# Performance work log

Measured on AMD Instinct MI355X. Metric: run time of the kernel, lower is better.

## Reference

```python
import jax, jax.numpy as jnp
import numpy as np

IN_F = 4096
OUT_F = 4096
GS = 128              # group_size
GC = IN_F // GS       # group_count = 32
PACK = 8              # int4 values per int32


def setup_inputs() -> dict:
    key = jax.random.key(0)
    k1, k2, k3, k4, k5 = jax.random.split(key, 5)
    x = jax.random.normal(k1, (4, 2048, IN_F), dtype=jnp.float32)
    # packed int4 weights: (out_features, in_features // 8), nibbles in low->high bits
    qweight = jax.random.randint(k2, (OUT_F, IN_F // PACK), -(2**31), 2**31 - 1, dtype=jnp.int32)
    scales = jax.random.uniform(k3, (GC, OUT_F), dtype=jnp.float32) * 0.01
    qzeros = jax.random.randint(k4, (GC, OUT_F), 0, 16, dtype=jnp.int32)
    bias = jax.random.normal(k5, (OUT_F,), dtype=jnp.float32) * 0.01
    return {"x": x, "qweight": qweight, "scales": scales, "qzeros": qzeros, "bias": bias}


def _dequantize(qweight, scales, qzeros):
    # unpack 8 nibbles per int32 along last dim (shifts 0,4,...,28), as in _unpack_int4_last_dim
    shifts = jnp.arange(0, 32, 4, dtype=jnp.int32)  # [8]
    w_int = ((qweight[:, :, None] >> shifts) & 15)  # (OUT, IN//8, 8)
    w_int = w_int.reshape(OUT_F, IN_F).astype(jnp.float32)  # (OUT, IN)
    gid = jnp.arange(IN_F) // GS  # (IN,) group id per input channel
    z = qzeros.astype(jnp.float32)[gid].T   # (OUT, IN)
    s = scales[gid].T                        # (OUT, IN)
    return (w_int - z) * s                   # (OUT, IN)


def reference(x, qweight, scales, qzeros, bias):
    W = _dequantize(qweight, scales, qzeros)          # (OUT, IN)
    # F.linear: y = x @ W^T + b
    return jnp.einsum('bsi,oi->bso', x, W) + bias
```

## Files before the change

### kernel.cpp

```cpp
#include <hip/hip_runtime.h>
#include <hip/hip_bf16.h>
#include <stdint.h>

#define IN_F 4096
#define OUT_F 4096
#define M_TOTAL 8192
#define NKT 64

typedef __hip_bfloat16 bf16;
typedef __attribute__((ext_vector_type(8))) short bf16x8;
typedef __attribute__((ext_vector_type(4))) float f32x4;

__global__ __launch_bounds__(256) void prep(const int* __restrict__ qweight,
                                            const float* __restrict__ scales,
                                            const int* __restrict__ qzeros,
                                            bf16* __restrict__ Wb,
                                            const float* __restrict__ x,
                                            bf16* __restrict__ Xb) {
    int b = blockIdx.x;
    if (b < 8192) {
        int idx = b * 256 + threadIdx.x;
        int o = idx >> 9;
        int j = idx & 511;
        int g = j >> 4;
        int qw = qweight[idx];
        float s = scales[g * OUT_F + o];
        float z = (float)qzeros[g * OUT_F + o];
        union { bf16 h[8]; uint4 q; } out;
#pragma unroll
        for (int k = 0; k < 8; ++k) {
            float w = (float)((qw >> (4 * k)) & 15);
            out.h[k] = __float2bfloat16((w - z) * s);
        }
        *reinterpret_cast<uint4*>(Wb + ((size_t)o * IN_F + j * 8)) = out.q;
    } else {
        int idx = (b - 8192) * 256 + threadIdx.x;
        const float4* p = reinterpret_cast<const float4*>(x) + (size_t)idx * 2;
        float4 a = p[0], c = p[1];
        union { bf16 h[8]; uint4 q; } o;
        o.h[0] = __float2bfloat16(a.x); o.h[1] = __float2bfloat16(a.y);
        o.h[2] = __float2bfloat16(a.z); o.h[3] = __float2bfloat16(a.w);
        o.h[4] = __float2bfloat16(c.x); o.h[5] = __float2bfloat16(c.y);
        o.h[6] = __float2bfloat16(c.z); o.h[7] = __float2bfloat16(c.w);
        reinterpret_cast<uint4*>(Xb)[idx] = o.q;
    }
}


__device__ __forceinline__ void gload16(const bf16* g, char* l) {
    __builtin_amdgcn_global_load_lds(
        (const __attribute__((address_space(1))) void*)g,
        (__attribute__((address_space(3))) void*)l, 16, 0, 0);
}

__device__ __forceinline__ void stage_half(const bf16* __restrict__ Gt,
                                           char* ldsb, int wave, int lane) {
    const int slog8 = ((lane & 7) ^ (lane >> 3)) * 8;
#pragma unroll
    for (int j = 0; j < 2; ++j) {
        int r = wave * 16 + j * 8 + (lane >> 3);
        gload16(Gt + (size_t)r * IN_F + slog8, ldsb + (wave * 2 + j) * 1024);
    }
}

#define BARRIER() do { asm volatile("" ::: "memory"); \
                       __builtin_amdgcn_s_barrier();  \
                       asm volatile("" ::: "memory"); } while (0)
#define LGKM0()   asm volatile("s_waitcnt lgkmcnt(0)" ::: "memory")
#define VMCNT6()  asm volatile("s_waitcnt vmcnt(6)" ::: "memory")
#define VMCNT0()  asm volatile("s_waitcnt vmcnt(0)" ::: "memory")

#define LDA_SET(DST, BUF, MH) do {                                              \
  _Pragma("unroll") for (int m4 = 0; m4 < 4; ++m4)                              \
  _Pragma("unroll") for (int kk = 0; kk < 2; ++kk)                              \
    DST[m4][kk] = *reinterpret_cast<const bf16x8*>(sm + (BUF) * 65536           \
        + (((MH) * 128 + wr * 64 + m4 * 16 + l15) << 7)                         \
        + ((((kk << 2) + lq) ^ l7) << 4));                                      \
} while (0)

#define LDB_SET(DST, BUF, NH) do {                                              \
  _Pragma("unroll") for (int n2 = 0; n2 < 2; ++n2)                              \
  _Pragma("unroll") for (int kk = 0; kk < 2; ++kk)                              \
    DST[n2][kk] = *reinterpret_cast<const bf16x8*>(sm + (BUF) * 65536 + 32768   \
        + (((NH) * 128 + wc * 32 + n2 * 16 + l15) << 7)                         \
        + ((((kk << 2) + lq) ^ l7) << 4));                                      \
} while (0)

#define MMA_Q(AF, BFR, MH, NH) do {                                             \
  __builtin_amdgcn_s_setprio(1);                                                \
  _Pragma("unroll") for (int m4 = 0; m4 < 4; ++m4)                              \
  _Pragma("unroll") for (int n2 = 0; n2 < 2; ++n2)                              \
  _Pragma("unroll") for (int kk = 0; kk < 2; ++kk)                              \
    acc[(MH) * 4 + m4][(NH) * 2 + n2] = __builtin_amdgcn_mfma_f32_16x16x32_bf16(\
        AF[m4][kk], BFR[n2][kk], acc[(MH) * 4 + m4][(NH) * 2 + n2], 0, 0, 0);   \
  __builtin_amdgcn_s_setprio(0);                                                \
} while (0)

__global__ __launch_bounds__(512, 2) void gemm256(const bf16* __restrict__ A,
                                                  const bf16* __restrict__ B,
                                                  const float* __restrict__ bias,
                                                  float* __restrict__ C) {
    extern __shared__ char sm[];
    const int tid  = threadIdx.x;
    const int wave = tid >> 6;
    const int lane = tid & 63;
    const int wr   = wave >> 2;
    const int wc   = wave & 3;
    const int l15  = lane & 15;
    const int lq   = lane >> 4;
    const int l7   = lane & 7;

    const int nwg = gridDim.x;
    const int cpx = nwg >> 3;
    const int wg  = blockIdx.x;
    const int swz = (wg & 7) * cpx + (wg >> 3);
    const int bm  = swz >> 4;
    const int bn  = swz & 15;
    const int m0  = bm * 256;
    const int n0  = bn * 256;

    const bf16* A0 = A + (size_t)m0 * IN_F;
    const bf16* A1 = A + (size_t)(m0 + 128) * IN_F;
    const bf16* B0 = B + (size_t)n0 * IN_F;
    const bf16* B1 = B + (size_t)(n0 + 128) * IN_F;

    f32x4 acc[8][4];
#pragma unroll
    for (int m = 0; m < 8; ++m)
#pragma unroll
        for (int n = 0; n < 4; ++n) acc[m][n] = (f32x4){0.f, 0.f, 0.f, 0.f};

    bf16x8 af0[4][2], af1[4][2], bfr0[2][2], bfr1[2][2];

    stage_half(A0,      sm + 0,     wave, lane);
    stage_half(A1,      sm + 16384, wave, lane);
    stage_half(B0,      sm + 32768, wave, lane);
    stage_half(B1,      sm + 49152, wave, lane);
    stage_half(A0 + 64, sm + 65536, wave, lane);
    stage_half(A1 + 64, sm + 81920, wave, lane);
    stage_half(B0 + 64, sm + 98304, wave, lane);
    VMCNT6();
    BARRIER();
    LDA_SET(af0, 0, 0);
    LDB_SET(bfr0, 0, 0);

    for (int i = 0; i < 32; ++i) {
        const int t1 = 2 * i + 1;
        const int t2 = 2 * i + 2;
        const int t3 = 2 * i + 3;
        const bool gg = (i < 31);

        stage_half(B1 + t1 * 64, sm + 114688, wave, lane);
        LGKM0();
        MMA_Q(af0, bfr0, 0, 0);
        LDA_SET(af1, 0, 1);
        BARRIER();
        if (gg) stage_half(A0 + t2 * 64, sm + 0, wave, lane);
        LGKM0();
        MMA_Q(af1, bfr0, 1, 0);
        LDB_SET(bfr1, 0, 1);
        BARRIER();
        if (gg) stage_half(A1 + t2 * 64, sm + 16384, wave, lane);
        LGKM0();
        MMA_Q(af0, bfr1, 0, 1);
        BARRIER();
        if (gg) stage_half(B0 + t2 * 64, sm + 32768, wave, lane);
        LGKM0();
        MMA_Q(af1, bfr1, 1, 1);
        if (gg) { VMCNT6(); } else { VMCNT0(); }
        LDA_SET(af0, 1, 0);
        LDB_SET(bfr0, 1, 0);
        BARRIER();

        if (gg) stage_half(B1 + t2 * 64, sm + 49152, wave, lane);
        LGKM0();
        MMA_Q(af0, bfr0, 0, 0);
        LDA_SET(af1, 1, 1);
        BARRIER();
        if (gg) stage_half(A0 + t3 * 64, sm + 65536, wave, lane);
        LGKM0();
        MMA_Q(af1, bfr0, 1, 0);
        LDB_SET(bfr1, 1, 1);
        BARRIER();
        if (gg) stage_half(A1 + t3 * 64, sm + 81920, wave, lane);
        LGKM0();
        MMA_Q(af0, bfr1, 0, 1);
        BARRIER();
        if (gg) stage_half(B0 + t3 * 64, sm + 98304, wave, lane);
        LGKM0();
        MMA_Q(af1, bfr1, 1, 1);
        if (gg) { VMCNT6(); } else { VMCNT0(); }
        if (gg) {
            LDA_SET(af0, 0, 0);
            LDB_SET(bfr0, 0, 0);
        }
        BARRIER();
    }

    const int crow_base = m0 + wr * 64 + lq * 4;
    const int ccol_base = n0 + wc * 32 + l15;
#pragma unroll
    for (int n = 0; n < 4; ++n) {
        const int NH = n >> 1, n2 = n & 1;
        const int col = ccol_base + NH * 128 + n2 * 16;
        float bv = bias[col];
#pragma unroll
        for (int m = 0; m < 8; ++m) {
            const int MH = m >> 2, m4 = m & 3;
            const int row = crow_base + MH * 128 + m4 * 16;
#pragma unroll
            for (int r = 0; r < 4; ++r)
                C[(size_t)(row + r) * OUT_F + col] = acc[m][n][r] + bv;
        }
    }
}

__global__ __launch_bounds__(256) void fallback_gemm(const float* __restrict__ x,
                                                     const int* __restrict__ qweight,
                                                     const float* __restrict__ scales,
                                                     const int* __restrict__ qzeros,
                                                     const float* __restrict__ bias,
                                                     float* __restrict__ out) {
    __shared__ float Asf[64][65];
    __shared__ float Bsf[64][65];
    int bm = blockIdx.x >> 6;
    int bn = blockIdx.x & 63;
    int m0 = bm * 64, n0 = bn * 64;
    int t  = threadIdx.x;
    int tr = t >> 4, tc = t & 15;
    float acc[4][4] = {};
    for (int kt = 0; kt < IN_F; kt += 64) {
#pragma unroll
        for (int i = 0; i < 4; ++i) {
            int idx = t + i * 256;
            int r = idx >> 4, c4 = idx & 15;
            float4 v = *reinterpret_cast<const float4*>(x + (size_t)(m0 + r) * IN_F + kt + c4 * 4);
            Asf[r][c4 * 4 + 0] = v.x; Asf[r][c4 * 4 + 1] = v.y;
            Asf[r][c4 * 4 + 2] = v.z; Asf[r][c4 * 4 + 3] = v.w;
        }
#pragma unroll
        for (int i = 0; i < 2; ++i) {
            int idx = t + i * 256;
            int r = idx >> 3, k8 = idx & 7;
            int kk = kt + k8 * 8;
            int o  = n0 + r;
            int qw = qweight[(size_t)o * (IN_F / 8) + (kk >> 3)];
            int g  = kk >> 7;
            float s = scales[g * OUT_F + o];
            float z = (float)qzeros[g * OUT_F + o];
#pragma unroll
            for (int b = 0; b < 8; ++b)
                Bsf[r][k8 * 8 + b] = ((float)((qw >> (4 * b)) & 15) - z) * s;
        }
        __syncthreads();
#pragma unroll 8
        for (int k = 0; k < 64; ++k) {
            float a[4], bb[4];
#pragma unroll
            for (int i = 0; i < 4; ++i) a[i] = Asf[tr * 4 + i][k];
#pragma unroll
            for (int j = 0; j < 4; ++j) bb[j] = Bsf[tc * 4 + j][k];
#pragma unroll
            for (int i = 0; i < 4; ++i)
#pragma unroll
                for (int j = 0; j < 4; ++j) acc[i][j] += a[i] * bb[j];
        }
        __syncthreads();
    }
#pragma unroll
    for (int i = 0; i < 4; ++i) {
        int row = m0 + tr * 4 + i;
#pragma unroll
        for (int j = 0; j < 4; ++j) {
            int col = n0 + tc * 4 + j;
            out[(size_t)row * OUT_F + col] = acc[i][j] + bias[col];
        }
    }
}

extern "C" void kernel_launch(void* const* d_in, const int* in_sizes, int n_in,
                              void* d_out, int out_size, void* d_ws, size_t ws_size,
                              hipStream_t stream) {
    (void)in_sizes; (void)n_in; (void)out_size;
    const float* x       = (const float*)d_in[0];
    const int*   qweight = (const int*)d_in[1];
    const float* scales  = (const float*)d_in[2];
    const int*   qzeros  = (const int*)d_in[3];
    const float* bias    = (const float*)d_in[4];
    float* out = (float*)d_out;

    const size_t needW = (size_t)OUT_F * IN_F * sizeof(bf16);
    const size_t needX = (size_t)M_TOTAL * IN_F * sizeof(bf16);

    if (ws_size >= needW + needX) {
        bf16* Wb = (bf16*)d_ws;
        bf16* Xb = (bf16*)((char*)d_ws + needW);
        prep<<<8192 + 16384, 256, 0, stream>>>(qweight, scales, qzeros, Wb, x, Xb);
        gemm256<<<(M_TOTAL / 256) * (OUT_F / 256), 512, 131072, stream>>>(Xb, Wb, bias, out);
    } else {
        fallback_gemm<<<(M_TOTAL / 64) * (OUT_F / 64), 256, 0, stream>>>(
            x, qweight, scales, qzeros, bias, out);
    }
}
```

Baseline: 268.8 us.

## Restructure GEMM main loop into two phases per k-tile with fewer barriers

Each k-tile now runs two MFMA phases, one per B half, instead of four quarter phases. Both A halves are loaded into registers up front, and the three next-tile global loads are issued together after one barrier. The vmcnt wait thresholds change to match the new load grouping, and s_setprio now brackets 32 MFMAs instead of 16. The goal is to halve the barriers per k-tile and give the scheduler longer MFMA runs. The cost is more live fragment registers and burstier global load issue.

```diff
diff --git a/kernel.cpp b/kernel.cpp
--- a/kernel.cpp
+++ b/kernel.cpp
@@ -67,7 +67,9 @@
                        __builtin_amdgcn_s_barrier();  \
                        asm volatile("" ::: "memory"); } while (0)
 #define LGKM0()   asm volatile("s_waitcnt lgkmcnt(0)" ::: "memory")
+#define VMCNT8()  asm volatile("s_waitcnt vmcnt(8)" ::: "memory")
 #define VMCNT6()  asm volatile("s_waitcnt vmcnt(6)" ::: "memory")
+#define VMCNT2()  asm volatile("s_waitcnt vmcnt(2)" ::: "memory")
 #define VMCNT0()  asm volatile("s_waitcnt vmcnt(0)" ::: "memory")
 
 #define LDA_SET(DST, BUF, MH) do {                                              \
@@ -87,12 +89,17 @@
 } while (0)
 
 #define MMA_Q(AF, BFR, MH, NH) do {                                             \
-  __builtin_amdgcn_s_setprio(1);                                                \
   _Pragma("unroll") for (int m4 = 0; m4 < 4; ++m4)                              \
   _Pragma("unroll") for (int n2 = 0; n2 < 2; ++n2)                              \
   _Pragma("unroll") for (int kk = 0; kk < 2; ++kk)                              \
     acc[(MH) * 4 + m4][(NH) * 2 + n2] = __builtin_amdgcn_mfma_f32_16x16x32_bf16(\
         AF[m4][kk], BFR[n2][kk], acc[(MH) * 4 + m4][(NH) * 2 + n2], 0, 0, 0);   \
+  } while (0)
+
+#define MMA_PH(BFR, NH) do {                                                    \
+  __builtin_amdgcn_s_setprio(1);                                                \
+  MMA_Q(af0, BFR, 0, NH);                                                       \
+  MMA_Q(af1, BFR, 1, NH);                                                       \
   __builtin_amdgcn_s_setprio(0);                                                \
 } while (0)
 
@@ -142,6 +149,7 @@
     VMCNT6();
     BARRIER();
     LDA_SET(af0, 0, 0);
+    LDA_SET(af1, 0, 1);
     LDB_SET(bfr0, 0, 0);
 
     for (int i = 0; i < 32; ++i) {
@@ -152,46 +160,42 @@
 
         stage_half(B1 + t1 * 64, sm + 114688, wave, lane);
         LGKM0();
-        MMA_Q(af0, bfr0, 0, 0);
-        LDA_SET(af1, 0, 1);
-        BARRIER();
-        if (gg) stage_half(A0 + t2 * 64, sm + 0, wave, lane);
-        LGKM0();
-        MMA_Q(af1, bfr0, 1, 0);
+        MMA_PH(bfr0, 0);
+        VMCNT8();
         LDB_SET(bfr1, 0, 1);
         BARRIER();
-        if (gg) stage_half(A1 + t2 * 64, sm + 16384, wave, lane);
+
+        if (gg) {
+            stage_half(A0 + t2 * 64, sm + 0,     wave, lane);
+            stage_half(A1 + t2 * 64, sm + 16384, wave, lane);
+            stage_half(B0 + t2 * 64, sm + 32768, wave, lane);
+        }
         LGKM0();
-        MMA_Q(af0, bfr1, 0, 1);
-        BARRIER();
-        if (gg) stage_half(B0 + t2 * 64, sm + 32768, wave, lane);
-        LGKM0();
-        MMA_Q(af1, bfr1, 1, 1);
-        if (gg) { VMCNT6(); } else { VMCNT0(); }
+        MMA_PH(bfr1, 1);
+        if (gg) { VMCNT8(); } else { VMCNT2(); }
         LDA_SET(af0, 1, 0);
+        LDA_SET(af1, 1, 1);
         LDB_SET(bfr0, 1, 0);
         BARRIER();
 
         if (gg) stage_half(B1 + t2 * 64, sm + 49152, wave, lane);
         LGKM0();
-        MMA_Q(af0, bfr0, 0, 0);
-        LDA_SET(af1, 1, 1);
-        BARRIER();
-        if (gg) stage_half(A0 + t3 * 64, sm + 65536, wave, lane);
-        LGKM0();
-        MMA_Q(af1, bfr0, 1, 0);
+        MMA_PH(bfr0, 0);
+        if (gg) { VMCNT8(); } else { VMCNT0(); }
         LDB_SET(bfr1, 1, 1);
         BARRIER();
-        if (gg) stage_half(A1 + t3 * 64, sm + 81920, wave, lane);
+
+        if (gg) {
+            stage_half(A0 + t3 * 64, sm + 65536, wave, lane);
+            stage_half(A1 + t3 * 64, sm + 81920, wave, lane);
+            stage_half(B0 + t3 * 64, sm + 98304, wave, lane);
+        }
         LGKM0();
-        MMA_Q(af0, bfr1, 0, 1);
-        BARRIER();
-        if (gg) stage_half(B0 + t3 * 64, sm + 98304, wave, lane);
-        LGKM0();
-        MMA_Q(af1, bfr1, 1, 1);
-        if (gg) { VMCNT6(); } else { VMCNT0(); }
+        MMA_PH(bfr1, 1);
         if (gg) {
+            VMCNT8();
             LDA_SET(af0, 0, 0);
+            LDA_SET(af1, 0, 1);
             LDB_SET(bfr0, 0, 0);
         }
         BARRIER();
```

Result: no change. 272.4 us (+1.3%).

## Double-buffer MFMA register fragments and use partial lgkmcnt/vmcnt waits

Applied to the files above, without the earlier changes.

Splits the A/B register fragments into two sets so LDS reads for the next quarter-step are issued earlier, and replaces full lgkmcnt(0) waits with partial counts (4/8/12). Global-load waits are tightened to vmcnt(4) at more points. The aim is to overlap LDS-to-register traffic with MFMA execution. In exchange it raises VGPR pressure, which could lower occupancy or cause spills, and the hand-tuned wait counts are fragile, so a wrong count risks reading stale data.

```diff
diff --git a/kernel.cpp b/kernel.cpp
--- a/kernel.cpp
+++ b/kernel.cpp
@@ -66,8 +66,12 @@
 #define BARRIER() do { asm volatile("" ::: "memory"); \
                        __builtin_amdgcn_s_barrier();  \
                        asm volatile("" ::: "memory"); } while (0)
-#define LGKM0()   asm volatile("s_waitcnt lgkmcnt(0)" ::: "memory")
+#define LGKM0()   asm volatile("s_waitcnt lgkmcnt(0)"  ::: "memory")
+#define LGKM4()   asm volatile("s_waitcnt lgkmcnt(4)"  ::: "memory")
+#define LGKM8()   asm volatile("s_waitcnt lgkmcnt(8)"  ::: "memory")
+#define LGKM12()  asm volatile("s_waitcnt lgkmcnt(12)" ::: "memory")
 #define VMCNT6()  asm volatile("s_waitcnt vmcnt(6)" ::: "memory")
+#define VMCNT4()  asm volatile("s_waitcnt vmcnt(4)" ::: "memory")
 #define VMCNT0()  asm volatile("s_waitcnt vmcnt(0)" ::: "memory")
 
 #define LDA_SET(DST, BUF, MH) do {                                              \
@@ -130,7 +134,8 @@
 #pragma unroll
         for (int n = 0; n < 4; ++n) acc[m][n] = (f32x4){0.f, 0.f, 0.f, 0.f};
 
-    bf16x8 af0[4][2], af1[4][2], bfr0[2][2], bfr1[2][2];
+    bf16x8 af0A[4][2], af1A[4][2], af0B[4][2], af1B[4][2];
+    bf16x8 bfr0A[2][2], bfr1A[2][2], bfr0B[2][2], bfr1B[2][2];
 
     stage_half(A0,      sm + 0,     wave, lane);
     stage_half(A1,      sm + 16384, wave, lane);
@@ -141,8 +146,9 @@
     stage_half(B0 + 64, sm + 98304, wave, lane);
     VMCNT6();
     BARRIER();
-    LDA_SET(af0, 0, 0);
-    LDB_SET(bfr0, 0, 0);
+    LDA_SET(af0A, 0, 0);
+    LDB_SET(bfr0A, 0, 0);
+    LDA_SET(af1A, 0, 1);
 
     for (int i = 0; i < 32; ++i) {
         const int t1 = 2 * i + 1;
@@ -151,49 +157,52 @@
         const bool gg = (i < 31);
 
         stage_half(B1 + t1 * 64, sm + 114688, wave, lane);
-        LGKM0();
-        MMA_Q(af0, bfr0, 0, 0);
-        LDA_SET(af1, 0, 1);
+        LGKM8();
+        MMA_Q(af0A, bfr0A, 0, 0);
+        VMCNT4();
+        LDB_SET(bfr1A, 0, 1);
         BARRIER();
         if (gg) stage_half(A0 + t2 * 64, sm + 0, wave, lane);
-        LGKM0();
-        MMA_Q(af1, bfr0, 1, 0);
-        LDB_SET(bfr1, 0, 1);
+        LGKM4();
+        MMA_Q(af1A, bfr0A, 1, 0);
+        VMCNT4();
         BARRIER();
         if (gg) stage_half(A1 + t2 * 64, sm + 16384, wave, lane);
         LGKM0();
-        MMA_Q(af0, bfr1, 0, 1);
+        MMA_Q(af0A, bfr1A, 0, 1);
+        if (gg) { VMCNT4(); } else { VMCNT0(); }
+        LDA_SET(af0B, 1, 0);
+        LDB_SET(bfr0B, 1, 0);
         BARRIER();
         if (gg) stage_half(B0 + t2 * 64, sm + 32768, wave, lane);
-        LGKM0();
-        MMA_Q(af1, bfr1, 1, 1);
-        if (gg) { VMCNT6(); } else { VMCNT0(); }
-        LDA_SET(af0, 1, 0);
-        LDB_SET(bfr0, 1, 0);
+        LGKM12();
+        MMA_Q(af1A, bfr1A, 1, 1);
+        VMCNT4();
+        LDA_SET(af1B, 1, 1);
         BARRIER();
 
         if (gg) stage_half(B1 + t2 * 64, sm + 49152, wave, lane);
-        LGKM0();
-        MMA_Q(af0, bfr0, 0, 0);
-        LDA_SET(af1, 1, 1);
+        LGKM8();
+        MMA_Q(af0B, bfr0B, 0, 0);
+        VMCNT4();
+        LDB_SET(bfr1B, 1, 1);
         BARRIER();
         if (gg) stage_half(A0 + t3 * 64, sm + 65536, wave, lane);
-        LGKM0();
-        MMA_Q(af1, bfr0, 1, 0);
-        LDB_SET(bfr1, 1, 1);
+        LGKM4();
+        MMA_Q(af1B, bfr0B, 1, 0);
+        VMCNT4();
         BARRIER();
         if (gg) stage_half(A1 + t3 * 64, sm + 81920, wave, lane);
         LGKM0();
-        MMA_Q(af0, bfr1, 0, 1);
+        MMA_Q(af0B, bfr1B, 0, 1);
+        VMCNT4();
+        if (gg) { LDA_SET(af0A, 0, 0); LDB_SET(bfr0A, 0, 0); }
         BARRIER();
         if (gg) stage_half(B0 + t3 * 64, sm + 98304, wave, lane);
-        LGKM0();
-        MMA_Q(af1, bfr1, 1, 1);
-        if (gg) { VMCNT6(); } else { VMCNT0(); }
-        if (gg) {
-            LDA_SET(af0, 0, 0);
-            LDB_SET(bfr0, 0, 0);
-        }
+        LGKM12();
+        MMA_Q(af1B, bfr1B, 1, 1);
+        VMCNT4();
+        if (gg) LDA_SET(af1A, 0, 1);
         BARRIER();
     }
 
```

Result: slower. 501.3 us (+86.5%).
